# Kernel optimization log

Measured on AMD Instinct MI355X. Metric: run time of the kernel, lower is better.

Reference implementation:

```python
import jax, jax.numpy as jnp
import numpy as np

N_QUBITS = 8


def setup_inputs() -> dict:
    key = jax.random.key(0)
    k1, k2, k3, k4 = jax.random.split(key, 4)
    B, S, E, F = 4, 4096, 1024, 4096
    x = jax.random.normal(k1, (B, S, E), dtype=jnp.float32)
    theta = jax.random.normal(k2, (N_QUBITS,), dtype=jnp.float32)
    # nn.Linear default init scale ~ 1/sqrt(fan_in)
    w1 = jax.random.normal(k3, (F, N_QUBITS), dtype=jnp.float32) / np.sqrt(N_QUBITS)
    w2 = jax.random.normal(k4, (E, F), dtype=jnp.float32) / np.sqrt(F)
    return {"x": x, "theta": theta, "w1": w1, "w2": w2}


def reference(x, theta, w1, w2):
    # Quantum circuit per wire i: |0> -RX(x_i)-> -RY(theta_i)-> <Z>
    # No entangling gates, so <Z_i> = cos(x_i) * cos(theta_i) exactly.
    q_vecs = jnp.cos(x[..., :N_QUBITS]) * jnp.cos(theta)  # [B,S,nq]
    h = jax.nn.relu(jnp.einsum('bsq,fq->bsf', q_vecs, w1))  # [B,S,F]
    # dropout is identity in eval mode
    out = jnp.einsum('bsf,ef->bse', h, w2)  # [B,S,E]
    return out
```

## Files before the change

### kernel.cpp

```cpp
#include <hip/hip_runtime.h>
#include <hip/hip_bf16.h>


#define M_TOTAL 16384
#define E_DIM 1024
#define F_DIM 4096
#define NQ 8

typedef __attribute__((ext_vector_type(8))) short bf16x8;
typedef __attribute__((ext_vector_type(8))) unsigned short ushort8;
typedef __attribute__((ext_vector_type(4))) float f32x4;

__device__ __forceinline__ unsigned short f2bf(float f) {
  union { float f; unsigned u; } c; c.f = f;
  unsigned u = c.u + (0x7fffu + ((c.u >> 16) & 1u));
  return (unsigned short)(u >> 16);
}

__global__ __launch_bounds__(256) void w2cvt_kernel(
    const float* __restrict__ w2, unsigned short* __restrict__ w2bf) {
  size_t i = ((size_t)blockIdx.x * 256 + threadIdx.x) * 8;
  float v[8];
  *(float4*)&v[0] = *(const float4*)&w2[i];
  *(float4*)&v[4] = *(const float4*)&w2[i + 4];
  ushort8 p;
#pragma unroll
  for (int j = 0; j < 8; ++j) p[j] = f2bf(v[j]);
  *(ushort8*)&w2bf[i] = p;
}

__global__ __launch_bounds__(256) void qrelu_kernel(
    const float* __restrict__ x, const float* __restrict__ theta,
    const float* __restrict__ w1, unsigned short* __restrict__ A, int m_base) {
  __shared__ float qv[32][NQ];
  const int t = threadIdx.x;
  const int m0 = m_base + blockIdx.x * 32;
  {
    const int ml = t >> 3, q = t & 7;
    float xv = x[(size_t)(m0 + ml) * 1024 + q];
    qv[ml][q] = cosf(xv) * cosf(theta[q]);
  }
  __syncthreads();

  for (int oi = 0; oi < 2; ++oi) {
    const int o = t + oi * 256;
    float w[64];
#pragma unroll
    for (int i = 0; i < 16; ++i)
      *(float4*)&w[i * 4] = *(const float4*)&w1[o * 64 + i * 4];
    for (int ml = 0; ml < 32; ++ml) {
      ushort8 pk;
#pragma unroll
      for (int j = 0; j < 8; ++j) {
        float s = 0.f;
#pragma unroll
        for (int q = 0; q < NQ; ++q) s = fmaf(qv[ml][q], w[j * 8 + q], s);
        pk[j] = f2bf(s > 0.f ? s : 0.f);
      }
      *(ushort8*)&A[(size_t)(m0 - m_base + ml) * F_DIM + o * 8] = pk;
    }
  }
}

#define MFMA_PHASE(ms, ns, B) do { \
  __builtin_amdgcn_s_barrier(); \
  asm volatile("s_waitcnt lgkmcnt(0)" ::: "memory"); \
  __builtin_amdgcn_sched_barrier(0); \
  __builtin_amdgcn_s_setprio(1); \
  _Pragma("unroll") \
  for (int mt2 = 0; mt2 < 4; ++mt2) { \
    _Pragma("unroll") \
    for (int nt2 = 0; nt2 < 2; ++nt2) { \
      _Pragma("unroll") \
      for (int kk = 0; kk < 2; ++kk) { \
        acc[(ms) * 4 + mt2][(ns) * 2 + nt2] = \
            __builtin_amdgcn_mfma_f32_16x16x32_bf16( \
                af[mt2][kk], B[nt2][kk], acc[(ms) * 4 + mt2][(ns) * 2 + nt2], \
                0, 0, 0); \
      } } } \
  __builtin_amdgcn_s_setprio(0); \
  __builtin_amdgcn_s_barrier(); \
} while (0)

__global__ __launch_bounds__(512, 2) void gemm8_kernel(
    const unsigned short* __restrict__ Abf, const unsigned short* __restrict__ w2bf,
    float* __restrict__ out, int m_base) {
  __shared__ __align__(16) unsigned short As[2][2][128 * 64];
  __shared__ __align__(16) unsigned short Bs[2][2][128 * 64];

  const int tid = threadIdx.x;
  const int lane = tid & 63;
  const int wid = tid >> 6;
  const int wr = wid >> 2;
  const int wc = wid & 3;

  const int nwg = gridDim.x;
  const int bid = blockIdx.x;
  const int qq = nwg >> 3, rr = nwg & 7;
  const int xcd = bid & 7, sub = bid >> 3;
  const int wgid =
      (xcd < rr ? xcd * (qq + 1) : rr * (qq + 1) + (xcd - rr) * qq) + sub;
  const int mb = wgid >> 2;
  const int nb = wgid & 3;

  const unsigned short* Ag = Abf + (size_t)mb * 256 * F_DIM;
  const unsigned short* Bg = w2bf + (size_t)nb * 256 * F_DIM;

  f32x4 acc[8][4] = {};
  bf16x8 af[4][2], blo[2][2], bhi[2][2];

  auto stA = [&](int buf, int half, int kt) {
#pragma unroll
    for (int rnd = 0; rnd < 2; ++rnd) {
      const int row = rnd * 64 + (tid >> 3);
      const int c = (tid & 7) ^ ((tid >> 3) & 7);
      const unsigned short* g =
          Ag + (size_t)(half * 128 + row) * F_DIM + kt * 64 + c * 8;
      __builtin_amdgcn_global_load_lds(
          (const __attribute__((address_space(1))) void*)g,
          (__attribute__((address_space(3))) void*)&As[buf][half]
                                                      [rnd * 4096 + wid * 512],
          16, 0, 0);
    }
  };
  auto stB = [&](int buf, int half, int kt) {
#pragma unroll
    for (int rnd = 0; rnd < 2; ++rnd) {
      const int row = rnd * 64 + (tid >> 3);
      const int c = (tid & 7) ^ ((tid >> 3) & 7);
      const unsigned short* g =
          Bg + (size_t)(half * 128 + row) * F_DIM + kt * 64 + c * 8;
      __builtin_amdgcn_global_load_lds(
          (const __attribute__((address_space(1))) void*)g,
          (__attribute__((address_space(3))) void*)&Bs[buf][half]
                                                      [rnd * 4096 + wid * 512],
          16, 0, 0);
    }
  };

  auto rdA = [&](int buf, int ms) {
#pragma unroll
    for (int mt2 = 0; mt2 < 4; ++mt2)
#pragma unroll
      for (int kk = 0; kk < 2; ++kk) {
        const int r = ms * 64 + mt2 * 16 + (lane & 15);
        const int c = (kk * 4 + (lane >> 4)) ^ (lane & 7);
        af[mt2][kk] = *(const bf16x8*)&As[buf][wr][r * 64 + c * 8];
      }
  };
  auto rdB = [&](int buf, int ns, bf16x8(&B)[2][2]) {
#pragma unroll
    for (int nt2 = 0; nt2 < 2; ++nt2)
#pragma unroll
      for (int kk = 0; kk < 2; ++kk) {
        const int rf = wc * 64 + ns * 32 + nt2 * 16 + (lane & 15);
        const int c = (kk * 4 + (lane >> 4)) ^ (lane & 7);
        B[nt2][kk] = *(const bf16x8*)&Bs[buf][rf >> 7][(rf & 127) * 64 + c * 8];
      }
  };

  stB(0, 0, 0); stB(0, 1, 0); stA(0, 0, 0); stA(0, 1, 0);
  stB(1, 0, 1); stB(1, 1, 1);
  asm volatile("s_waitcnt vmcnt(4)" ::: "memory");
  __builtin_amdgcn_s_barrier();

#pragma unroll 1
  for (int it = 0; it < F_DIM / 128; ++it) {
    const bool last = (it == F_DIM / 128 - 1);
    const int k0 = 2 * it;
    rdA(0, 0); rdB(0, 0, blo);
    stA(1, 0, k0 + 1);
    MFMA_PHASE(0, 0, blo);
    rdB(0, 1, bhi);
    stA(1, 1, k0 + 1);
    MFMA_PHASE(0, 1, bhi);
    rdA(0, 1);
    if (!last) stB(0, 0, k0 + 2);
    MFMA_PHASE(1, 1, bhi);
    if (!last) {
      stB(0, 1, k0 + 2);
      asm volatile("s_waitcnt vmcnt(4)" ::: "memory");
    } else {
      asm volatile("s_waitcnt vmcnt(0)" ::: "memory");
    }
    MFMA_PHASE(1, 0, blo);
    rdA(1, 0); rdB(1, 0, blo);
    if (!last) stA(0, 0, k0 + 2);
    MFMA_PHASE(0, 0, blo);
    rdB(1, 1, bhi);
    if (!last) stA(0, 1, k0 + 2);
    MFMA_PHASE(0, 1, bhi);
    rdA(1, 1);
    if (!last) stB(1, 0, k0 + 3);
    MFMA_PHASE(1, 1, bhi);
    if (!last) {
      stB(1, 1, k0 + 3);
      asm volatile("s_waitcnt vmcnt(4)" ::: "memory");
    }
    MFMA_PHASE(1, 0, blo);
  }

  const int cl = lane & 15, rg = lane >> 4;
  float* ob = out + (size_t)(m_base + mb * 256 + wr * 128) * E_DIM + nb * 256 +
              wc * 64 + cl;
#pragma unroll
  for (int mt = 0; mt < 8; ++mt)
#pragma unroll
    for (int r = 0; r < 4; ++r) {
      float* orow = ob + (size_t)(mt * 16 + rg * 4 + r) * E_DIM;
#pragma unroll
      for (int nt = 0; nt < 4; ++nt) orow[nt * 16] = acc[mt][nt][r];
    }
}

extern "C" void kernel_launch(void* const* d_in, const int* in_sizes, int n_in,
                              void* d_out, int out_size, void* d_ws, size_t ws_size,
                              hipStream_t stream) {
  const float* x = (const float*)d_in[0];
  const float* theta = (const float*)d_in[1];
  const float* w1 = (const float*)d_in[2];
  const float* w2 = (const float*)d_in[3];
  float* out = (float*)d_out;

  unsigned short* w2bf = (unsigned short*)d_ws;
  unsigned short* A = w2bf + (size_t)E_DIM * F_DIM;

  size_t abytes = ws_size - (size_t)E_DIM * F_DIM * 2;
  size_t maxrows = abytes / ((size_t)F_DIM * 2);
  int Mc = (int)((maxrows / 256) * 256);
  if (Mc > M_TOTAL) Mc = M_TOTAL;
  if (Mc < 256) Mc = 256;

  w2cvt_kernel<<<E_DIM * F_DIM / 2048, 256, 0, stream>>>(w2, w2bf);

  for (int mb = 0; mb < M_TOTAL; mb += Mc) {
    int rows = M_TOTAL - mb < Mc ? M_TOTAL - mb : Mc;
    qrelu_kernel<<<rows / 32, 256, 0, stream>>>(x, theta, w1, A, mb);
    gemm8_kernel<<<(rows / 256) * 4, 512, 0, stream>>>(A, w2bf, out, mb);
  }
}
```

Baseline: 155.5 us.

## Restructure GEMM prefetch schedule with pointer-increment loads and partial LDS waits

Moves global-to-LDS loads to run earlier: three half-tiles are prefetched in the prologue and each stage issues three loads, waiting with vmcnt(6) instead of vmcnt(4). Global addresses are now held as running pointers advanced by 64 elements, and LDS read offsets are precomputed, which removes per-call address arithmetic. Both B fragments of a stage are read up front and the first MFMA phase waits only on a partial lgkmcnt, so LDS reads overlap MFMAs. The cost is more loads in flight and extra register pressure from the hoisted B reads and the eight pointers.

```diff
diff --git a/kernel.cpp b/kernel.cpp
--- a/kernel.cpp
+++ b/kernel.cpp
@@ -62,9 +62,9 @@
   }
 }
 
-#define MFMA_PHASE(ms, ns, B) do { \
+#define PHASE(ms, ns, B, W) do { \
   __builtin_amdgcn_s_barrier(); \
-  asm volatile("s_waitcnt lgkmcnt(0)" ::: "memory"); \
+  asm volatile("s_waitcnt lgkmcnt(" #W ")" ::: "memory"); \
   __builtin_amdgcn_sched_barrier(0); \
   __builtin_amdgcn_s_setprio(1); \
   _Pragma("unroll") \
@@ -82,6 +82,20 @@
   __builtin_amdgcn_s_barrier(); \
 } while (0)
 
+#define RD_A(buf, ms) do { \
+  _Pragma("unroll") \
+  for (int mt2 = 0; mt2 < 4; ++mt2) { \
+    af[mt2][0] = *(const bf16x8*)&asW[(buf) * 16384 + (ms) * 4096 + mt2 * 1024 + aO0]; \
+    af[mt2][1] = *(const bf16x8*)&asW[(buf) * 16384 + (ms) * 4096 + mt2 * 1024 + aO1]; \
+  } } while (0)
+
+#define RD_B(buf, ns, B) do { \
+  _Pragma("unroll") \
+  for (int nt2 = 0; nt2 < 2; ++nt2) { \
+    B[nt2][0] = *(const bf16x8*)&bsW[(buf) * 16384 + (ns) * 2048 + nt2 * 1024 + bO0]; \
+    B[nt2][1] = *(const bf16x8*)&bsW[(buf) * 16384 + (ns) * 2048 + nt2 * 1024 + bO1]; \
+  } } while (0)
+
 __global__ __launch_bounds__(512, 2) void gemm8_kernel(
     const unsigned short* __restrict__ Abf, const unsigned short* __restrict__ w2bf,
     float* __restrict__ out, int m_base) {
@@ -109,95 +123,86 @@
   f32x4 acc[8][4] = {};
   bf16x8 af[4][2], blo[2][2], bhi[2][2];
 
-  auto stA = [&](int buf, int half, int kt) {
-#pragma unroll
-    for (int rnd = 0; rnd < 2; ++rnd) {
-      const int row = rnd * 64 + (tid >> 3);
-      const int c = (tid & 7) ^ ((tid >> 3) & 7);
-      const unsigned short* g =
-          Ag + (size_t)(half * 128 + row) * F_DIM + kt * 64 + c * 8;
-      __builtin_amdgcn_global_load_lds(
-          (const __attribute__((address_space(1))) void*)g,
-          (__attribute__((address_space(3))) void*)&As[buf][half]
-                                                      [rnd * 4096 + wid * 512],
-          16, 0, 0);
-    }
+  const int hi4 = lane >> 4, l7 = lane & 7, l15 = lane & 15;
+  const int aO0 = l15 * 64 + ((hi4 ^ l7) << 3);
+  const int aO1 = aO0 ^ 32;
+  const int bO0 = ((wc & 1) * 64 + l15) * 64 + ((hi4 ^ l7) << 3);
+  const int bO1 = bO0 ^ 32;
+  const unsigned short* asW = &As[0][wr][0];
+  const unsigned short* bsW = &Bs[0][wc >> 1][0];
+
+  const int srow = tid >> 3;
+  const int sc = (tid & 7) ^ (srow & 7);
+  const unsigned short* pA0 = Ag + (size_t)(srow)*F_DIM + sc * 8;
+  const unsigned short* pA1 = Ag + (size_t)(64 + srow) * F_DIM + sc * 8;
+  const unsigned short* pA2 = Ag + (size_t)(128 + srow) * F_DIM + sc * 8;
+  const unsigned short* pA3 = Ag + (size_t)(192 + srow) * F_DIM + sc * 8;
+  const unsigned short* pB0 = Bg + (size_t)(srow)*F_DIM + sc * 8;
+  const unsigned short* pB1 = Bg + (size_t)(64 + srow) * F_DIM + sc * 8;
+  const unsigned short* pB2 = Bg + (size_t)(128 + srow) * F_DIM + sc * 8;
+  const unsigned short* pB3 = Bg + (size_t)(192 + srow) * F_DIM + sc * 8;
+
+  auto stA = [&](int buf, int half, const unsigned short*& r0,
+                 const unsigned short*& r1) {
+    unsigned short* d = &As[buf][half][wid * 512];
+    __builtin_amdgcn_global_load_lds(
+        (const __attribute__((address_space(1))) void*)r0,
+        (__attribute__((address_space(3))) void*)d, 16, 0, 0);
+    __builtin_amdgcn_global_load_lds(
+        (const __attribute__((address_space(1))) void*)r1,
+        (__attribute__((address_space(3))) void*)(d + 4096), 16, 0, 0);
+    r0 += 64; r1 += 64;
   };
-  auto stB = [&](int buf, int half, int kt) {
-#pragma unroll
-    for (int rnd = 0; rnd < 2; ++rnd) {
-      const int row = rnd * 64 + (tid >> 3);
-      const int c = (tid & 7) ^ ((tid >> 3) & 7);
-      const unsigned short* g =
-          Bg + (size_t)(half * 128 + row) * F_DIM + kt * 64 + c * 8;
-      __builtin_amdgcn_global_load_lds(
-          (const __attribute__((address_space(1))) void*)g,
-          (__attribute__((address_space(3))) void*)&Bs[buf][half]
-                                                      [rnd * 4096 + wid * 512],
-          16, 0, 0);
-    }
+  auto stB = [&](int buf, int half, const unsigned short*& r0,
+                 const unsigned short*& r1) {
+    unsigned short* d = &Bs[buf][half][wid * 512];
+    __builtin_amdgcn_global_load_lds(
+        (const __attribute__((address_space(1))) void*)r0,
+        (__attribute__((address_space(3))) void*)d, 16, 0, 0);
+    __builtin_amdgcn_global_load_lds(
+        (const __attribute__((address_space(1))) void*)r1,
+        (__attribute__((address_space(3))) void*)(d + 4096), 16, 0, 0);
+    r0 += 64; r1 += 64;
   };
 
-  auto rdA = [&](int buf, int ms) {
-#pragma unroll
-    for (int mt2 = 0; mt2 < 4; ++mt2)
-#pragma unroll
-      for (int kk = 0; kk < 2; ++kk) {
-        const int r = ms * 64 + mt2 * 16 + (lane & 15);
-        const int c = (kk * 4 + (lane >> 4)) ^ (lane & 7);
-        af[mt2][kk] = *(const bf16x8*)&As[buf][wr][r * 64 + c * 8];
-      }
-  };
-  auto rdB = [&](int buf, int ns, bf16x8(&B)[2][2]) {
-#pragma unroll
-    for (int nt2 = 0; nt2 < 2; ++nt2)
-#pragma unroll
-      for (int kk = 0; kk < 2; ++kk) {
-        const int rf = wc * 64 + ns * 32 + nt2 * 16 + (lane & 15);
-        const int c = (kk * 4 + (lane >> 4)) ^ (lane & 7);
-        B[nt2][kk] = *(const bf16x8*)&Bs[buf][rf >> 7][(rf & 127) * 64 + c * 8];
-      }
-  };
-
-  stB(0, 0, 0); stB(0, 1, 0); stA(0, 0, 0); stA(0, 1, 0);
-  stB(1, 0, 1); stB(1, 1, 1);
-  asm volatile("s_waitcnt vmcnt(4)" ::: "memory");
+  stB(0, 0, pB0, pB1); stB(0, 1, pB2, pB3);
+  stA(0, 0, pA0, pA1); stA(0, 1, pA2, pA3);
+  stB(1, 0, pB0, pB1); stB(1, 1, pB2, pB3);
+  stA(1, 0, pA0, pA1);
+  asm volatile("s_waitcnt vmcnt(6)" ::: "memory");
   __builtin_amdgcn_s_barrier();
 
 #pragma unroll 1
   for (int it = 0; it < F_DIM / 128; ++it) {
-    const bool last = (it == F_DIM / 128 - 1);
-    const int k0 = 2 * it;
-    rdA(0, 0); rdB(0, 0, blo);
-    stA(1, 0, k0 + 1);
-    MFMA_PHASE(0, 0, blo);
-    rdB(0, 1, bhi);
-    stA(1, 1, k0 + 1);
-    MFMA_PHASE(0, 1, bhi);
-    rdA(0, 1);
-    if (!last) stB(0, 0, k0 + 2);
-    MFMA_PHASE(1, 1, bhi);
-    if (!last) {
-      stB(0, 1, k0 + 2);
-      asm volatile("s_waitcnt vmcnt(4)" ::: "memory");
+    const bool notlast = (it != F_DIM / 128 - 1);
+    RD_A(0, 0); RD_B(0, 0, blo); RD_B(0, 1, bhi);
+    stA(1, 1, pA2, pA3);
+    PHASE(0, 0, blo, 4);
+    PHASE(0, 1, bhi, 0);
+    RD_A(0, 1);
+    if (notlast) stB(0, 0, pB0, pB1);
+    PHASE(1, 1, bhi, 0);
+    if (notlast) {
+      stB(0, 1, pB2, pB3);
+      stA(0, 0, pA0, pA1);
+      asm volatile("s_waitcnt vmcnt(6)" ::: "memory");
     } else {
       asm volatile("s_waitcnt vmcnt(0)" ::: "memory");
     }
-    MFMA_PHASE(1, 0, blo);
-    rdA(1, 0); rdB(1, 0, blo);
-    if (!last) stA(0, 0, k0 + 2);
-    MFMA_PHASE(0, 0, blo);
-    rdB(1, 1, bhi);
-    if (!last) stA(0, 1, k0 + 2);
-    MFMA_PHASE(0, 1, bhi);
-    rdA(1, 1);
-    if (!last) stB(1, 0, k0 + 3);
-    MFMA_PHASE(1, 1, bhi);
-    if (!last) {
-      stB(1, 1, k0 + 3);
-      asm volatile("s_waitcnt vmcnt(4)" ::: "memory");
-    }
-    MFMA_PHASE(1, 0, blo);
+    PHASE(1, 0, blo, 0);
+    RD_A(1, 0); RD_B(1, 0, blo); RD_B(1, 1, bhi);
+    if (notlast) stA(0, 1, pA2, pA3);
+    PHASE(0, 0, blo, 4);
+    PHASE(0, 1, bhi, 0);
+    RD_A(1, 1);
+    if (notlast) stB(1, 0, pB0, pB1);
+    PHASE(1, 1, bhi, 0);
+    if (notlast) {
+      stB(1, 1, pB2, pB3);
+      stA(1, 0, pA0, pA1);
+      asm volatile("s_waitcnt vmcnt(6)" ::: "memory");
+    }
+    PHASE(1, 0, blo, 0);
   }
 
   const int cl = lane & 15, rg = lane >> 4;
```

Result: slower. 167.3 us (+7.6%).
